# Kernel optimization log

Hardware: AMD Instinct MI355X
Metric: run time of the kernel (lower is better)

## Reference

```python
import jax, jax.numpy as jnp
import numpy as np

K = 5   # reassembly kernel size
G = 1   # group size
S = 2   # upsample scale factor


def setup_inputs() -> dict:
    key = jax.random.key(0)
    kf, km = jax.random.split(key)
    N, C, H, W = 4, 256, 64, 64
    features = jax.random.normal(kf, (N, C, H, W), dtype=jnp.float32)
    # masks: [N, K*K*G, H*S, W*S]; CARAFE masks are non-negative (softmax-normalized upstream)
    masks = jax.random.uniform(km, (N, K * K * G, H * S, W * S), dtype=jnp.float32)
    return {"features": features, "masks": masks}


def _carafe(features, masks, k=K, g=G, s=S):
    # features: [N, C, H, W]; masks: [N, k*k*g, H*s, W*s]
    N, C, H, W = features.shape
    pad = (k - 1) // 2
    fp = jnp.pad(features, ((0, 0), (0, 0), (pad, pad), (pad, pad)))
    # unfold k x k neighborhoods at LOW resolution: [N, C, k*k, H, W]
    patches = jnp.stack(
        [fp[:, :, i:i + H, j:j + W] for i in range(k) for j in range(k)], axis=2
    )
    cg = C // g
    patches = patches.reshape(N, g, cg, k * k, H, W)
    # mask channel layout is [group, k*k]; split output pixels (i = h*s + p)
    m = masks.reshape(N, g, k * k, H, s, W, s)
    # out[n,g,c,h,p,w,q] = sum_k m[n,g,k,h,p,w,q] * patches[n,g,c,k,h,w]
    out = jnp.einsum('ngkhpwq,ngckhw->ngchpwq', m, patches)
    return out.reshape(N, C, H * s, W * s)


def reference(features, masks):
    return _carafe(features, masks)
```

## Files before the change

### kernel.cpp

```cpp
#include <hip/hip_runtime.h>


#define CN 4
#define CC 256
#define CH 64
#define CW 64
#define CK 5
#define OH 128
#define OW 128

constexpr int TILE = 16;
constexpr int SROWS = TILE + 4;
constexpr int SCOLS = TILE + 4;
constexpr int LSTR  = 24;
constexpr int LBUF  = SROWS * LSTR;
constexpr int CH_PER_BLOCK = 32;

__global__ __launch_bounds__(256, 2)
void carafe_kernel(const float* __restrict__ feat,
                   const float* __restrict__ masks,
                   float* __restrict__ out)
{
    __shared__ float lds[2 * LBUF];

    const int tid  = threadIdx.x;
    const int wloc = tid & 15;
    const int hloc = tid >> 4;

    const int w0 = blockIdx.x * TILE;
    const int h0 = blockIdx.y * TILE;
    const int z  = blockIdx.z;
    const int n  = z >> 3;
    const int c0 = (z & 7) * CH_PER_BLOCK;

    const int r0 = tid / SCOLS, q0 = tid % SCOLS;
    const int gr0 = h0 - 2 + r0, gc0 = w0 - 2 + q0;
    const bool val0 = (gr0 >= 0) & (gr0 < CH) & (gc0 >= 0) & (gc0 < CW);
    const int off0 = val0 ? (gr0 * CW + gc0) : 0;
    const int l0   = r0 * LSTR + q0;

    const int e1 = tid + 256;
    const bool has1 = e1 < SROWS * SCOLS;
    const int r1 = e1 / SCOLS, q1 = e1 % SCOLS;
    const int gr1 = h0 - 2 + r1, gc1 = w0 - 2 + q1;
    const bool val1 = has1 & (gr1 >= 0) & (gr1 < CH) & (gc1 >= 0) & (gc1 < CW);
    const int off1 = val1 ? (gr1 * CW + gc1) : 0;
    const int l1   = r1 * LSTR + q1;

    const float* fbase = feat + (size_t)(n * CC + c0) * (CH * CW);

    const int oh0 = 2 * (h0 + hloc);
    const int ow0 = 2 * (w0 + wloc);
    const float* mp = masks + (((size_t)n * (CK * CK)) * OH + oh0) * OW + ow0;
    float2 m0[25], m1[25];
#pragma unroll
    for (int t = 0; t < 25; ++t) {
        m0[t] = *(const float2*)(mp + (size_t)t * (OH * OW));
        m1[t] = *(const float2*)(mp + (size_t)t * (OH * OW) + OW);
    }

    float pa, pb;
    pa = val0 ? fbase[off0] : 0.0f;
    pb = val1 ? fbase[(size_t)CH * CW + 0 + off1] : 0.0f;
    pa = val0 ? fbase[off0] : 0.0f;
    pb = val1 ? fbase[off1] : 0.0f;
    lds[l0] = pa;
    if (has1) lds[l1] = pb;
    pa = val0 ? fbase[1 * (CH * CW) + off0] : 0.0f;
    pb = val1 ? fbase[1 * (CH * CW) + off1] : 0.0f;

    float* obase = out + (((size_t)(n * CC + c0) * OH + oh0) * OW + ow0);

    for (int ci = 0; ci < CH_PER_BLOCK; ++ci) {
        __syncthreads();

        if (ci + 1 < CH_PER_BLOCK) {
            float* dst = &lds[((ci + 1) & 1) * LBUF];
            dst[l0] = pa;
            if (has1) dst[l1] = pb;
        }
        if (ci + 2 < CH_PER_BLOCK) {
            const float* fc = fbase + (size_t)(ci + 2) * (CH * CW);
            pa = val0 ? fc[off0] : 0.0f;
            pb = val1 ? fc[off1] : 0.0f;
        }

        const float* lb = &lds[(ci & 1) * LBUF + hloc * LSTR + wloc];
        float a00 = 0.f, a01 = 0.f, a10 = 0.f, a11 = 0.f;
#pragma unroll
        for (int i = 0; i < CK; ++i) {
#pragma unroll
            for (int j = 0; j < CK; ++j) {
                const int t = i * CK + j;
                const float f = lb[i * LSTR + j];
                a00 += m0[t].x * f;
                a01 += m0[t].y * f;
                a10 += m1[t].x * f;
                a11 += m1[t].y * f;
            }
        }

        float* op = obase + (size_t)ci * (OH * OW);
        *(float2*)op          = make_float2(a00, a01);
        *(float2*)(op + OW)   = make_float2(a10, a11);
    }
}

extern "C" void kernel_launch(void* const* d_in, const int* in_sizes, int n_in,
                              void* d_out, int out_size, void* d_ws, size_t ws_size,
                              hipStream_t stream) {
    const float* feat  = (const float*)d_in[0];
    const float* masks = (const float*)d_in[1];
    float* out = (float*)d_out;

    dim3 grid(CW / TILE, CH / TILE, CN * (CC / CH_PER_BLOCK));
    dim3 block(256);
    hipLaunchKernelGGL(carafe_kernel, grid, block, 0, stream, feat, masks, out);
}
```

Baseline: 111.1 us.

## Stage four channels per barrier with channel-interleaved float2 LDS and nontemporal stores

```diff
diff --git a/kernel.cpp b/kernel.cpp
--- a/kernel.cpp
+++ b/kernel.cpp
@@ -9,19 +9,23 @@
 #define OH 128
 #define OW 128
 
-constexpr int TILE = 16;
+typedef float f32x2 __attribute__((ext_vector_type(2)));
+
+constexpr int TILE  = 16;
 constexpr int SROWS = TILE + 4;
-constexpr int SCOLS = TILE + 4;
 constexpr int LSTR  = 24;
 constexpr int LBUF  = SROWS * LSTR;
+constexpr int CPB   = 4;
+constexpr int PPS   = CPB / 2;
 constexpr int CH_PER_BLOCK = 32;
+constexpr int NSTG  = CH_PER_BLOCK / CPB;
 
 __global__ __launch_bounds__(256, 2)
 void carafe_kernel(const float* __restrict__ feat,
                    const float* __restrict__ masks,
                    float* __restrict__ out)
 {
-    __shared__ float lds[2 * LBUF];
+    __shared__ float2 lds[2 * PPS * LBUF];
 
     const int tid  = threadIdx.x;
     const int wloc = tid & 15;
@@ -33,19 +37,14 @@
     const int n  = z >> 3;
     const int c0 = (z & 7) * CH_PER_BLOCK;
 
-    const int r0 = tid / SCOLS, q0 = tid % SCOLS;
-    const int gr0 = h0 - 2 + r0, gc0 = w0 - 2 + q0;
-    const bool val0 = (gr0 >= 0) & (gr0 < CH) & (gc0 >= 0) & (gc0 < CW);
-    const int off0 = val0 ? (gr0 * CW + gc0) : 0;
-    const int l0   = r0 * LSTR + q0;
-
-    const int e1 = tid + 256;
-    const bool has1 = e1 < SROWS * SCOLS;
-    const int r1 = e1 / SCOLS, q1 = e1 % SCOLS;
-    const int gr1 = h0 - 2 + r1, gc1 = w0 - 2 + q1;
-    const bool val1 = has1 & (gr1 >= 0) & (gr1 < CH) & (gc1 >= 0) & (gc1 < CW);
-    const int off1 = val1 ? (gr1 * CW + gc1) : 0;
-    const int l1   = r1 * LSTR + q1;
+    const int r  = tid / 10;
+    const int pc = tid % 10;
+    const int q  = 2 * pc;
+    const int gr = h0 - 2 + r;
+    const int gc = w0 - 2 + q;
+    const bool sv = (tid < 200) & (gr >= 0) & (gr < CH) & (gc >= 0) & (gc <= CW - 2);
+    const int goff = sv ? (gr * CW + gc) : 0;
+    const int l    = r * LSTR + q;
 
     const float* fbase = feat + (size_t)(n * CC + c0) * (CH * CW);
 
@@ -59,50 +58,64 @@
         m1[t] = *(const float2*)(mp + (size_t)t * (OH * OW) + OW);
     }
 
-    float pa, pb;
-    pa = val0 ? fbase[off0] : 0.0f;
-    pb = val1 ? fbase[(size_t)CH * CW + 0 + off1] : 0.0f;
-    pa = val0 ? fbase[off0] : 0.0f;
-    pb = val1 ? fbase[off1] : 0.0f;
-    lds[l0] = pa;
-    if (has1) lds[l1] = pb;
-    pa = val0 ? fbase[1 * (CH * CW) + off0] : 0.0f;
-    pb = val1 ? fbase[1 * (CH * CW) + off1] : 0.0f;
+    float2 pa[PPS], pb[PPS];
+
+    auto loadStage = [&](int s) {
+#pragma unroll
+        for (int p = 0; p < PPS; ++p) {
+            const float* f0 = fbase + (size_t)(s * CPB + 2 * p) * (CH * CW);
+            pa[p] = sv ? *(const float2*)(f0 + goff) : make_float2(0.f, 0.f);
+            pb[p] = sv ? *(const float2*)(f0 + CH * CW + goff) : make_float2(0.f, 0.f);
+        }
+    };
+    auto writeStage = [&](int buf) {
+        if (tid < 200) {
+            float2* dst = &lds[buf * (PPS * LBUF)];
+#pragma unroll
+            for (int p = 0; p < PPS; ++p) {
+                dst[p * LBUF + l]     = make_float2(pa[p].x, pb[p].x);
+                dst[p * LBUF + l + 1] = make_float2(pa[p].y, pb[p].y);
+            }
+        }
+    };
+
+    loadStage(0);
+    writeStage(0);
+    loadStage(1);
 
     float* obase = out + (((size_t)(n * CC + c0) * OH + oh0) * OW + ow0);
 
-    for (int ci = 0; ci < CH_PER_BLOCK; ++ci) {
+    for (int s = 0; s < NSTG; ++s) {
         __syncthreads();
 
-        if (ci + 1 < CH_PER_BLOCK) {
-            float* dst = &lds[((ci + 1) & 1) * LBUF];
-            dst[l0] = pa;
-            if (has1) dst[l1] = pb;
+        if (s + 1 < NSTG) writeStage((s + 1) & 1);
+        if (s + 2 < NSTG) loadStage(s + 2);
+
+        const float2* sb = &lds[(s & 1) * (PPS * LBUF)];
+#pragma unroll
+        for (int p = 0; p < PPS; ++p) {
+            const float2* lb = sb + p * LBUF + hloc * LSTR + wloc;
+            float a00 = 0.f, a01 = 0.f, a10 = 0.f, a11 = 0.f;
+            float b00 = 0.f, b01 = 0.f, b10 = 0.f, b11 = 0.f;
+#pragma unroll
+            for (int i = 0; i < CK; ++i) {
+#pragma unroll
+                for (int j = 0; j < CK; ++j) {
+                    const int t = i * CK + j;
+                    const float2 f = lb[i * LSTR + j];
+                    a00 += m0[t].x * f.x; a01 += m0[t].y * f.x;
+                    a10 += m1[t].x * f.x; a11 += m1[t].y * f.x;
+                    b00 += m0[t].x * f.y; b01 += m0[t].y * f.y;
+                    b10 += m1[t].x * f.y; b11 += m1[t].y * f.y;
+                }
+            }
+            float* op0 = obase + (size_t)(s * CPB + 2 * p) * (OH * OW);
+            float* op1 = op0 + (OH * OW);
+            __builtin_nontemporal_store((f32x2){a00, a01}, (f32x2*)op0);
+            __builtin_nontemporal_store((f32x2){a10, a11}, (f32x2*)(op0 + OW));
+            __builtin_nontemporal_store((f32x2){b00, b01}, (f32x2*)op1);
+            __builtin_nontemporal_store((f32x2){b10, b11}, (f32x2*)(op1 + OW));
         }
-        if (ci + 2 < CH_PER_BLOCK) {
-            const float* fc = fbase + (size_t)(ci + 2) * (CH * CW);
-            pa = val0 ? fc[off0] : 0.0f;
-            pb = val1 ? fc[off1] : 0.0f;
-        }
-
-        const float* lb = &lds[(ci & 1) * LBUF + hloc * LSTR + wloc];
-        float a00 = 0.f, a01 = 0.f, a10 = 0.f, a11 = 0.f;
-#pragma unroll
-        for (int i = 0; i < CK; ++i) {
-#pragma unroll
-            for (int j = 0; j < CK; ++j) {
-                const int t = i * CK + j;
-                const float f = lb[i * LSTR + j];
-                a00 += m0[t].x * f;
-                a01 += m0[t].y * f;
-                a10 += m1[t].x * f;
-                a11 += m1[t].y * f;
-            }
-        }
-
-        float* op = obase + (size_t)ci * (OH * OW);
-        *(float2*)op          = make_float2(a00, a01);
-        *(float2*)(op + OW)   = make_float2(a10, a11);
     }
 }
 
```

Result: faster. 105.5 us (-5.0%).
